# Optimization experiments

Hardware: AMD Instinct MI355X
Metric: run time of the kernel (lower is better)

The kernel has to match this reference:

```python
import jax, jax.numpy as jnp
import numpy as np

K = 40  # GravNetConv k (hardcoded in PFNet7.forward's conv1)

def lrelu(x):
    # LeakyReLU(negative_slope=0.5)
    return jnp.where(x >= 0, x, 0.5 * x)

def lin(x, W, b=None):
    y = x @ W
    return y + b if b is not None else y


def setup_inputs() -> dict:
    key = jax.random.key(0)
    ks = jax.random.split(key, 24)
    N = 16384
    inp = {}
    inp["x0"] = jax.random.normal(ks[0], (N, 12), jnp.float32)
    inp["ygen"] = jax.random.normal(ks[1], (N, 6), jnp.float32)
    inp["ycand"] = jax.random.normal(ks[2], (N, 6), jnp.float32)
    inp["ygen_id"] = jax.random.randint(ks[3], (N,), 0, 6)
    inp["ycand_id"] = jax.random.randint(ks[4], (N,), 0, 6)

    def lp(k, din, dout):  # torch Linear default init (uniform +/- 1/sqrt(fan_in))
        s = float(1.0 / np.sqrt(din))
        kw, kb = jax.random.split(k)
        W = jax.random.uniform(kw, (din, dout), jnp.float32, -s, s)
        b = jax.random.uniform(kb, (dout,), jnp.float32, -s, s)
        return W, b

    inp["n1W0"], inp["n1b0"] = lp(ks[5], 12, 64)
    inp["n1W1"], inp["n1b1"] = lp(ks[6], 64, 64)
    inp["n1W2"], inp["n1b2"] = lp(ks[7], 64, 12)
    # GravNetConv: lin_s (space, 8), lin_h (propagate, 22), lin_out (12 + 2*22 -> 64)
    inp["gWs"], inp["gbs"] = lp(ks[8], 12, 8)
    inp["gWh"], inp["gbh"] = lp(ks[9], 12, 22)
    inp["gWo"], inp["gbo"] = lp(ks[10], 56, 64)
    # GraphConv: lin_rel (with bias), lin_root (no bias, PyG convention)
    inp["c2Wrel"], inp["c2brel"] = lp(ks[11], 64, 64)
    inp["c2Wroot"] = lp(ks[12], 64, 64)[0]
    inp["n2W0"], inp["n2b0"] = lp(ks[13], 64, 126)
    inp["n2W1"], inp["n2b1"] = lp(ks[14], 126, 126)
    inp["n2W2"], inp["n2b2"] = lp(ks[15], 126, 126)
    inp["n2W3"], inp["n2b3"] = lp(ks[16], 126, 6)
    inp["n3W0"], inp["n3b0"] = lp(ks[17], 82, 126)
    inp["n3W1"], inp["n3b1"] = lp(ks[18], 126, 126)
    inp["n3W2"], inp["n3b2"] = lp(ks[19], 126, 126)
    inp["n3W3"], inp["n3b3"] = lp(ks[20], 126, 6)
    return inp


def reference(x0, ygen, ycand, ygen_id, ycand_id,
              n1W0, n1b0, n1W1, n1b1, n1W2, n1b2,
              gWs, gbs, gWh, gbh, gWo, gbo,
              c2Wrel, c2brel, c2Wroot,
              n2W0, n2b0, n2W1, n2b1, n2W2, n2b2, n2W3, n2b3,
              n3W0, n3b0, n3W1, n3b1, n3W2, n3b2, n3W3, n3b3):
    N = x0.shape[0]
    # nn1 encoder
    x = lrelu(lin(x0, n1W0, n1b0))
    x = lrelu(lin(x, n1W1, n1b1))
    x = lrelu(lin(x, n1W2, n1b2))            # [N,12]
    # ---- GravNetConv: dynamic kNN graph in learned 8-dim space ----
    s = lin(x, gWs, gbs)                     # [N,8] spatial coords
    h = lin(x, gWh, gbh)                     # [N,22] propagated features
    sq = jnp.sum(s * s, axis=1)
    d2 = sq[:, None] + sq[None, :] - 2.0 * (s @ s.T)   # [N,N] squared dists
    ar = jnp.arange(N)
    d2 = d2.at[ar, ar].set(jnp.inf)          # knn_graph loop=False: no self edges
    negd2, idx = jax.lax.top_k(-d2, K)       # [N,K] k nearest neighbors
    w = jnp.exp(10.0 * negd2)                # edge_weight = exp(-10 * d^2)
    msg = h[idx] * w[..., None]              # [N,K,22] gathered messages
    agg = jnp.concatenate([msg.mean(axis=1), msg.max(axis=1)], axis=-1)  # [N,44]
    x = lin(jnp.concatenate([agg, x], axis=-1), gWo, gbo)  # [N,64]
    # ---- GraphConv on the same kNN graph (add-aggregation, edge-weighted) ----
    nbr = jnp.sum(x[idx] * w[..., None], axis=1)  # [N,64]
    x = lin(nbr, c2Wrel, c2brel) + x @ c2Wroot     # [N,64]
    # nn2: class id head
    y = lrelu(lin(x, n2W0, n2b0))
    y = lrelu(lin(y, n2W1, n2b1))
    y = lrelu(lin(y, n2W2, n2b2))
    cand_ids = lrelu(lin(y, n2W3, n2b3))     # [N,6]
    z = jnp.concatenate([x, cand_ids, x0], axis=-1)  # [N,82]
    z = lrelu(lin(z, n3W0, n3b0))
    z = lrelu(lin(z, n3W1, n3b1))
    z = lrelu(lin(z, n3W2, n3b2))
    cand_p4 = lrelu(lin(z, n3W3, n3b3))      # [N,6]
    return (cand_ids, cand_p4, ygen_id, ygen, ycand_id, ycand)
```

## Files before the change

kernel.cpp:

```cpp
#include <hip/hip_runtime.h>
#include <math.h>

static constexpr int KNN = 40;

__device__ __forceinline__ float lrelu_f(float v){ return v >= 0.f ? v : 0.5f*v; }

typedef _Float16 half8 __attribute__((ext_vector_type(8)));
typedef float    f32x4 __attribute__((ext_vector_type(4)));

__device__ __forceinline__ void gload16(const void* g, void* l){
    __builtin_amdgcn_global_load_lds((const __attribute__((address_space(1))) void*)g,
                                     (__attribute__((address_space(3))) void*)l, 16, 0, 0);
}

#define PAD_OFF_GWS   0
#define PAD_OFF_GWH   192
#define PAD_OFF_N1W2  576
#define PAD_OFF_N2W3  1600
#define PAD_OFF_N3W3  3616
#define PAD_TOTAL     5632

#define T_N2W0  0
#define T_N2W1  8192
#define T_N2W2  24576
#define T_N3W0  40960
#define T_N3W1  53248
#define T_N3W2  69632
#define T_TOTAL 86016

__global__ void pad_all(const float* gWs,const float* gWh,const float* n1W2,
                        const float* n2W3,const float* n3W3,
                        const float* n2W0,const float* n2W1,const float* n2W2,
                        const float* n3W0,const float* n3W1,const float* n3W2,
                        float* __restrict__ wp, _Float16* __restrict__ wt)
{
    int i = blockIdx.x*blockDim.x + threadIdx.x;
    if (i < PAD_TOTAL) {
        const float* src; int cols, sh, off;
        if      (i < PAD_OFF_GWH)  { src=gWs;  cols=8;  sh=4; off=PAD_OFF_GWS;  }
        else if (i < PAD_OFF_N1W2) { src=gWh;  cols=22; sh=5; off=PAD_OFF_GWH;  }
        else if (i < PAD_OFF_N2W3) { src=n1W2; cols=12; sh=4; off=PAD_OFF_N1W2; }
        else if (i < PAD_OFF_N3W3) { src=n2W3; cols=6;  sh=4; off=PAD_OFF_N2W3; }
        else                       { src=n3W3; cols=6;  sh=4; off=PAD_OFF_N3W3; }
        int li = i - off;
        int r = li >> sh, c = li & ((1<<sh)-1);
        wp[i] = (c < cols) ? src[r*cols + c] : 0.f;
        return;
    }
    int j = i - PAD_TOTAL;
    if (j >= T_TOTAL) return;
    const float* src; int KP, K, off;
    if      (j < T_N2W1) { src=n2W0; KP=64;  K=64;  off=T_N2W0; }
    else if (j < T_N2W2) { src=n2W1; KP=128; K=126; off=T_N2W1; }
    else if (j < T_N3W0) { src=n2W2; KP=128; K=126; off=T_N2W2; }
    else if (j < T_N3W1) { src=n3W0; KP=96;  K=82;  off=T_N3W0; }
    else if (j < T_N3W2) { src=n3W1; KP=128; K=126; off=T_N3W1; }
    else                 { src=n3W2; KP=128; K=126; off=T_N3W2; }
    int li = j - off;
    int n = li / KP, k = li - n*KP;
    float v = (n < 126 && k < K) ? src[k*126 + n] : 0.f;
    wt[j] = (_Float16)v;
}

template<int K, int NOUT, int WPITCH, bool RELU, int NTH>
__device__ __forceinline__
void lin8(const float* __restrict__ Xs, int xpitch,
          const float* __restrict__ W, const float* __restrict__ Bv,
          float* __restrict__ Y, int ypitch, int tid)
{
    constexpr int NP  = ((NOUT+7)/8)*8;
    constexpr int NCG = NP/8;
    constexpr int NW  = NTH/64;
    const int lane = tid & 63;
    for (int g0 = tid >> 6; g0 < NCG; g0 += NW) {
        const int cg = __builtin_amdgcn_readfirstlane(g0);
        float acc[8];
        #pragma unroll
        for (int j=0;j<8;++j){ int c=cg*8+j; acc[j] = (c < NOUT) ? Bv[c] : 0.f; }
        const float* xrow = &Xs[(long)lane*xpitch];
        const float* wp = &W[cg*8];
        #pragma unroll 4
        for (int k=0;k<K;++k){
            const float xv = xrow[k];
            const float4* w4 = reinterpret_cast<const float4*>(wp + (long)k*WPITCH);
            float4 a = w4[0], b = w4[1];
            acc[0]=fmaf(xv,a.x,acc[0]); acc[1]=fmaf(xv,a.y,acc[1]);
            acc[2]=fmaf(xv,a.z,acc[2]); acc[3]=fmaf(xv,a.w,acc[3]);
            acc[4]=fmaf(xv,b.x,acc[4]); acc[5]=fmaf(xv,b.y,acc[5]);
            acc[6]=fmaf(xv,b.z,acc[6]); acc[7]=fmaf(xv,b.w,acc[7]);
        }
        #pragma unroll
        for (int j=0;j<8;++j){
            int c = cg*8 + j;
            if (c < NOUT){ float v = acc[j]; if (RELU) v = lrelu_f(v); Y[(long)lane*ypitch + c] = v; }
        }
    }
    __syncthreads();
}

template<int K, int NOUT, int WPITCH, int NTH>
__device__ __forceinline__
void lin8_dual(const float* __restrict__ Xs, int xp, const float* __restrict__ X2s, int xp2,
               const float* __restrict__ W, const float* __restrict__ Bv, const float* __restrict__ W2,
               float* __restrict__ Y, int ypitch, int tid)
{
    constexpr int NP  = ((NOUT+7)/8)*8;
    constexpr int NCG = NP/8;
    constexpr int NW  = NTH/64;
    const int lane = tid & 63;
    for (int g0 = tid >> 6; g0 < NCG; g0 += NW) {
        const int cg = __builtin_amdgcn_readfirstlane(g0);
        float acc[8];
        #pragma unroll
        for (int j=0;j<8;++j){ int c=cg*8+j; acc[j] = (c < NOUT) ? Bv[c] : 0.f; }
        {
            const float* xrow = &Xs[(long)lane*xp];
            const float* wp = &W[cg*8];
            #pragma unroll 4
            for (int k=0;k<K;++k){
                const float xv = xrow[k];
                const float4* w4 = reinterpret_cast<const float4*>(wp + (long)k*WPITCH);
                float4 a = w4[0], b = w4[1];
                acc[0]=fmaf(xv,a.x,acc[0]); acc[1]=fmaf(xv,a.y,acc[1]);
                acc[2]=fmaf(xv,a.z,acc[2]); acc[3]=fmaf(xv,a.w,acc[3]);
                acc[4]=fmaf(xv,b.x,acc[4]); acc[5]=fmaf(xv,b.y,acc[5]);
                acc[6]=fmaf(xv,b.z,acc[6]); acc[7]=fmaf(xv,b.w,acc[7]);
            }
        }
        {
            const float* xrow = &X2s[(long)lane*xp2];
            const float* wp = &W2[cg*8];
            #pragma unroll 4
            for (int k=0;k<K;++k){
                const float xv = xrow[k];
                const float4* w4 = reinterpret_cast<const float4*>(wp + (long)k*WPITCH);
                float4 a = w4[0], b = w4[1];
                acc[0]=fmaf(xv,a.x,acc[0]); acc[1]=fmaf(xv,a.y,acc[1]);
                acc[2]=fmaf(xv,a.z,acc[2]); acc[3]=fmaf(xv,a.w,acc[3]);
                acc[4]=fmaf(xv,b.x,acc[4]); acc[5]=fmaf(xv,b.y,acc[5]);
                acc[6]=fmaf(xv,b.z,acc[6]); acc[7]=fmaf(xv,b.w,acc[7]);
            }
        }
        #pragma unroll
        for (int j=0;j<8;++j){
            int c = cg*8 + j;
            if (c < NOUT) Y[(long)lane*ypitch + c] = acc[j];
        }
    }
    __syncthreads();
}

__global__ __launch_bounds__(512)
void f1_encoder(const float* __restrict__ x0, const float* __restrict__ wp,
                const float* n1W0,const float* n1b0,const float* n1W1,const float* n1b1,
                const float* n1b2, const float* gbs, const float* gbh,
                float* __restrict__ x12g,
                _Float16* __restrict__ SA16, _Float16* __restrict__ SB16 ,
                float* __restrict__ hg )
{
    __shared__ float A1[64*65], A2[64*65], Ss[64*9];
    const int tid = threadIdx.x;
    const long row0 = (long)blockIdx.x*64;
    lin8<12,64,64,true,512>(x0+row0*12,12, n1W0, n1b0, A1,65, tid);
    lin8<64,64,64,true,512>(A1,65, n1W1, n1b1, A2,65, tid);
    lin8<64,12,16,true,512>(A2,65, wp+PAD_OFF_N1W2, n1b2, A1,13, tid);
    for (int i=tid;i<64*12;i+=512){ int r=i/12,c=i-r*12; x12g[(row0+r)*12+c]=A1[r*13+c]; }
    lin8<12,8,16,false,512>(A1,13, wp+PAD_OFF_GWS, gbs, Ss,9, tid);
    lin8<12,22,32,false,512>(A1,13, wp+PAD_OFF_GWH, gbh, hg+row0*32,32, tid);
    if (tid < 64) {
        const long node = row0 + tid;
        float sv[8]; float nq = 0.f;
        #pragma unroll
        for (int k=0;k<8;++k){ float v=Ss[tid*9+k]; sv[k]=v; nq=fmaf(v,v,nq); }
        _Float16 ch[8], clo[8];
        #pragma unroll
        for (int k=0;k<8;++k){ ch[k]=(_Float16)sv[k]; clo[k]=(_Float16)(sv[k]-(float)ch[k]); }
        _Float16 nh = (_Float16)nq, nl = (_Float16)(nq-(float)nh);
        const _Float16 one = (_Float16)1.f, zero = (_Float16)0.f;
        half8 a0,a1,a2,b0,b2;
        #pragma unroll
        for (int k=0;k<8;++k){
            a0[k]=ch[k]; a1[k]=clo[k]; a2[k]=ch[k];
            b0[k]=(_Float16)(-2.f*(float)ch[k]);
            b2[k]=(_Float16)(-2.f*(float)clo[k]);
        }
        half8 a3 = {nh, nl, one, one, zero, zero, zero, zero};
        half8 b3 = {one, one, nh, nl, zero, zero, zero, zero};
        half8* ap = (half8*)&SA16[(size_t)node*32];
        ap[0]=a0; ap[1]=a1; ap[2]=a2; ap[3]=a3;
        half8* bp = (half8*)&SB16[(size_t)node*40];
        bp[0]=b0; bp[1]=b0; bp[2]=b2; bp[3]=b3;
        bp[4]=half8{zero,zero,zero,zero,zero,zero,zero,zero};
    }
}

template<int C>
__device__ __forceinline__ unsigned dpp_umin(unsigned x){
    unsigned y = (unsigned)__builtin_amdgcn_update_dpp((int)x, (int)x, C, 0xf, 0xf, false);
    return x < y ? x : y;
}
__device__ __forceinline__ unsigned wave_umin64(unsigned x){
    x = dpp_umin<0x111>(x);
    x = dpp_umin<0x112>(x);
    x = dpp_umin<0x114>(x);
    x = dpp_umin<0x118>(x);
    x = dpp_umin<0x142>(x);
    x = dpp_umin<0x143>(x);
    return x;
}
__device__ __forceinline__ unsigned med3_u32(unsigned a, unsigned b, unsigned c){
    unsigned d;
    asm("v_med3_u32 %0, %1, %2, %3" : "=v"(d) : "v"(a), "v"(b), "v"(c));
    return d;
}

__global__ __launch_bounds__(512)
void knn_scan(const _Float16* __restrict__ SA, const _Float16* __restrict__ SB,
              unsigned* __restrict__ part, int N)
{
    __shared__ __align__(16) _Float16 SBl[2][256*40];
    const int tid  = threadIdx.x;
    const int lane = tid & 63;
    const int w    = tid >> 6;
    const int g    = w >> 2, qt = w & 3;
    const int col  = lane & 15, kg = lane >> 4;
    const int qg   = blockIdx.x >> 1, half = blockIdx.x & 1;
    const int qb   = qg*32 + g*16;
    const int qtile = qb >> 8;
    const int rhs0  = (qb & 255) + kg*4;
    const int T0 = half*32;

    half8 afrag = *(const half8*)&SA[(size_t)(qb + col)*32 + kg*8];
    unsigned s0[4], s1[4];
    #pragma unroll
    for (int r=0;r<4;++r){ s0[r]=0xFFFFFFFFu; s1[r]=0xFFFFFFFFu; }

    {
        const char* gp = (const char*)(SB + (size_t)T0*256*40);
        gload16(gp + (size_t)tid*16,        &SBl[0][(size_t)tid*8]);
        gload16(gp + (size_t)(tid+512)*16,  &SBl[0][(size_t)(tid+512)*8]);
        if (tid < 256) gload16(gp + (size_t)(tid+1024)*16, &SBl[0][(size_t)(tid+1024)*8]);
    }
    __syncthreads();
    #pragma unroll 1
    for (int t = T0; t < T0+32; ++t) {
        const int cur = t & 1;
        if (t+1 < T0+32) {
            const char* gp = (const char*)(SB + (size_t)(t+1)*256*40);
            _Float16* lp = SBl[cur^1];
            gload16(gp + (size_t)tid*16,        &lp[(size_t)tid*8]);
            gload16(gp + (size_t)(tid+512)*16,  &lp[(size_t)(tid+512)*8]);
            if (tid < 256) gload16(gp + (size_t)(tid+1024)*16, &lp[(size_t)(tid+1024)*8]);
        }
        const _Float16* tb = SBl[cur];
        if (t != qtile) {
            #pragma unroll
            for (int c3=0;c3<4;++c3){
                const int cl_ = (qt*4+c3)*16 + col;
                half8 b = *(const half8*)&tb[cl_*40 + kg*8];
                f32x4 acc = {0.f,0.f,0.f,0.f};
                acc = __builtin_amdgcn_mfma_f32_16x16x32_f16(afrag, b, acc, 0, 0, 0);
                const unsigned ib = (unsigned)((t<<8)|cl_);
                #pragma unroll
                for (int r=0;r<4;++r){
                    float d2 = fmaxf(acc[r], 0.f);
                    unsigned key = (__float_as_uint(d2) & 0xFFFFC000u) | ib;
                    unsigned lo = s0[r] < key ? s0[r] : key;
                    s1[r] = med3_u32(s0[r], s1[r], key);
                    s0[r] = lo;
                }
            }
        } else {
            #pragma unroll
            for (int c3=0;c3<4;++c3){
                const int cl_ = (qt*4+c3)*16 + col;
                half8 b = *(const half8*)&tb[cl_*40 + kg*8];
                f32x4 acc = {0.f,0.f,0.f,0.f};
                acc = __builtin_amdgcn_mfma_f32_16x16x32_f16(afrag, b, acc, 0, 0, 0);
                const unsigned ib = (unsigned)((t<<8)|cl_);
                #pragma unroll
                for (int r=0;r<4;++r){
                    float d2 = fmaxf(acc[r], 0.f);
                    unsigned key = (__float_as_uint(d2) & 0xFFFFC000u) | ib;
                    if (cl_ == rhs0 + r) key = 0xFFFFFFFFu;
                    unsigned lo = s0[r] < key ? s0[r] : key;
                    s1[r] = med3_u32(s0[r], s1[r], key);
                    s0[r] = lo;
                }
            }
        }
        __syncthreads();
    }

    #pragma unroll
    for (int r=0;r<4;++r){
        const long q = (long)qg*32 + g*16 + kg*4 + r;
        unsigned* pp = &part[((size_t)q*2 + half)*128 + qt*32 + col*2];
        pp[0] = s0[r]; pp[1] = s1[r];
    }
}

__global__ __launch_bounds__(512)
void knn_merge(const unsigned* __restrict__ part,
               int* __restrict__ idx_out, float* __restrict__ w_out)
{
    const int lane = threadIdx.x & 63, w = threadIdx.x >> 6;
    const long q = (long)blockIdx.x*8 + w;
    const uint4 kk = *reinterpret_cast<const uint4*>(&part[(size_t)q*256 + lane*4]);
    unsigned k0=kk.x, k1=kk.y, k2=kk.z, k3=kk.w;
    unsigned saved = 0;
    #pragma unroll 1
    for (int p=0;p<KNN;++p){
        unsigned a = k0 < k1 ? k0 : k1;
        unsigned b = k2 < k3 ? k2 : k3;
        unsigned lmin = a < b ? a : b;
        unsigned red = wave_umin64(lmin);
        unsigned gm = (unsigned)__builtin_amdgcn_readlane((int)red, 63);
        unsigned long long bal = __ballot(lmin == gm);
        int owner = __ffsll((long long)bal) - 1;
        if (lane == owner){
            if      (k0 == gm) k0 = 0xFFFFFFFFu;
            else if (k1 == gm) k1 = 0xFFFFFFFFu;
            else if (k2 == gm) k2 = 0xFFFFFFFFu;
            else               k3 = 0xFFFFFFFFu;
        }
        if (lane == p) saved = gm;
    }
    if (lane < KNN){
        idx_out[q*KNN + lane] = (int)(saved & 16383u);
        const float d2 = __uint_as_float(saved & 0xFFFFC000u);
        w_out[q*KNN + lane] = expf(-10.f*d2);
    }
}

__global__ __launch_bounds__(512)
void f2_agg(const float* __restrict__ hg , const int* __restrict__ idx,
            const float* __restrict__ wgt, const float* __restrict__ x12g,
            const float* gWo, const float* gbo, float* __restrict__ xg)
{
    __shared__ int   IDs[64*40];
    __shared__ float Wt[64*40];
    __shared__ float AGG[64*57];
    const int tid = threadIdx.x;
    const long row0 = (long)blockIdx.x*64;
    for (int i=tid;i<64*40;i+=512){ int r=i/40,k=i-r*40;
        IDs[i]=idx[(row0+r)*40+k]; Wt[i]=wgt[(row0+r)*40+k]; }
    for (int i=tid;i<64*12;i+=512){ int r=i/12,c=i-r*12; AGG[r*57+44+c]=x12g[(row0+r)*12+c]; }
    __syncthreads();
    {
        const int r = tid & 63, g = tid >> 6;
        const int f0 = g*4;
        const int nf = (f0 < 22) ? ((22-f0) < 4 ? (22-f0) : 4) : 0;
        float sm[4], mx[4];
        #pragma unroll
        for (int u=0;u<4;++u){ sm[u]=0.f; mx[u]=-INFINITY; }
        if (nf > 0) {
            #pragma unroll 1
            for (int k=0;k<40;++k){
                int j = IDs[r*40+k]; float wv = Wt[r*40+k];
                float4 h0 = *reinterpret_cast<const float4*>(&hg[(long)j*32 + f0]);
                float hv[4] = {h0.x,h0.y,h0.z,h0.w};
                #pragma unroll
                for (int u=0;u<4;++u){ float m = hv[u]*wv; sm[u]+=m; mx[u]=fmaxf(mx[u],m); }
            }
            #pragma unroll
            for (int u=0;u<4;++u) if (u<nf){ AGG[r*57+f0+u]=sm[u]*(1.f/40.f); AGG[r*57+22+f0+u]=mx[u]; }
        }
    }
    __syncthreads();
    lin8<56,64,64,false,512>(AGG,57, gWo, gbo, xg+row0*64,64, tid);
}

template<int KP>
__device__ __forceinline__
void mfma_layer(const _Float16* __restrict__ Xl, const _Float16* __restrict__ WTg,
                _Float16* __restrict__ Wl,
                const float* __restrict__ Bv, _Float16* __restrict__ Yl, int tid)
{
    {
        const half8* src = reinterpret_cast<const half8*>(WTg);
        half8* dst = reinterpret_cast<half8*>(Wl);
        constexpr int CHUNKS = 128*KP/8;
        #pragma unroll
        for (int i = tid; i < CHUNKS; i += 1024) dst[i] = src[i];
    }
    __syncthreads();
    const int lane = tid & 63;
    const int wid  = __builtin_amdgcn_readfirstlane(tid >> 6);
    const int m   = wid & 3;
    const int nb  = wid >> 2;
    const int c15 = lane & 15;
    const int kg  = lane >> 4;
    f32x4 acc0 = {0.f,0.f,0.f,0.f};
    f32x4 acc1 = {0.f,0.f,0.f,0.f};
    const _Float16* xb = &Xl[(m*16 + c15)*136];
    const _Float16* w0 = &Wl[(nb*16 + c15)*KP];
    const _Float16* w1 = &Wl[((nb+4)*16 + c15)*KP];
    #pragma unroll
    for (int ks = 0; ks < KP/32; ++ks) {
        const int kb = kg*8 + ks*32;
        half8 a  = *reinterpret_cast<const half8*>(&xb[kb]);
        half8 b0 = *reinterpret_cast<const half8*>(&w0[kb]);
        half8 b1 = *reinterpret_cast<const half8*>(&w1[kb]);
        acc0 = __builtin_amdgcn_mfma_f32_16x16x32_f16(a, b0, acc0, 0, 0, 0);
        acc1 = __builtin_amdgcn_mfma_f32_16x16x32_f16(a, b1, acc1, 0, 0, 0);
    }
    const int drow = m*16 + kg*4;
    const int c0 = nb*16 + c15;
    const int c1 = (nb+4)*16 + c15;
    #pragma unroll
    for (int r = 0; r < 4; ++r) {
        float v0 = (c0 < 126) ? lrelu_f(acc0[r] + Bv[c0]) : 0.f;
        float v1 = (c1 < 126) ? lrelu_f(acc1[r] + Bv[c1]) : 0.f;
        Yl[(drow+r)*136 + c0] = (_Float16)v0;
        Yl[(drow+r)*136 + c1] = (_Float16)v1;
    }
    __syncthreads();
}

__device__ __forceinline__
void lin_out6h(const _Float16* __restrict__ Xs, const float* __restrict__ Wp,
               float* __restrict__ Wl6, const float* __restrict__ Bv,
               float* __restrict__ Y, int ypitch, int tid)
{
    for (int i = tid; i < 126*8; i += 1024) {
        int k = i >> 3, c = i & 7;
        Wl6[i] = Wp[k*16 + c];
    }
    __syncthreads();
    if (tid < 64*6) {
        const int r = tid / 6, c = tid - r*6;
        float acc = Bv[c];
        const _Float16* xrow = &Xs[r*136];
        #pragma unroll 4
        for (int k=0;k<126;++k) acc = fmaf((float)xrow[k], Wl6[k*8+c], acc);
        Y[(long)r*ypitch + c] = lrelu_f(acc);
    }
    __syncthreads();
}

__global__ __launch_bounds__(1024)
void f345(const float* __restrict__ xgin, const int* __restrict__ idx,
          const float* __restrict__ wgt,
          const float* c2Wrel, const float* c2brel, const float* c2Wroot,
          const float* __restrict__ x0,
          const float* __restrict__ wp, const _Float16* __restrict__ wt,
          const float* A_b0,const float* A_b1,const float* A_b2,const float* A_b3,
          const float* B_b0,const float* B_b1,const float* B_b2,const float* B_b3,
          float* __restrict__ outIds, float* __restrict__ outP4)
{
    __shared__ float XCs[64*65];
    __shared__ __align__(16) char uni[69120];
    int*   IDs = (int*)uni;
    float* Wt  = (float*)(uni+10240);
    float* NB  = (float*)(uni+20480);
    float* XGs = (float*)(uni+37120);
    _Float16* bufA = (_Float16*)uni;
    _Float16* bufB = (_Float16*)(uni+17408);
    _Float16* Wl   = (_Float16*)(uni+34816);
    float*    IDS6 = (float*)(uni+67584);

    const int tid = threadIdx.x;
    const long row0 = (long)blockIdx.x*64;
    for (int i=tid;i<64*40;i+=1024){ int r=i/40,k=i-r*40;
        IDs[i]=idx[(row0+r)*40+k]; Wt[i]=wgt[(row0+r)*40+k]; }
    for (int i=tid;i<64*64;i+=1024){ int r=i>>6,c=i&63; XGs[r*65+c]=xgin[(row0+r)*64+c]; }
    __syncthreads();
    {
        const int r = tid & 63, g = tid >> 6;
        float acc[4] = {0.f,0.f,0.f,0.f};
        #pragma unroll 1
        for (int k=0;k<40;++k){
            int j = IDs[r*40+k]; float wv = Wt[r*40+k];
            float4 v = *reinterpret_cast<const float4*>(&xgin[(long)j*64 + g*4]);
            acc[0]=fmaf(v.x,wv,acc[0]); acc[1]=fmaf(v.y,wv,acc[1]);
            acc[2]=fmaf(v.z,wv,acc[2]); acc[3]=fmaf(v.w,wv,acc[3]);
        }
        __syncthreads();
        #pragma unroll
        for (int j=0;j<4;++j) NB[r*65 + g*4 + j] = acc[j];
    }
    __syncthreads();
    lin8_dual<64,64,64,1024>(NB,65, XGs,65, c2Wrel,c2brel,c2Wroot, XCs,65, tid);
    for (int i=tid;i<64*64;i+=1024){ int r=i>>6,c=i&63;
        bufA[r*136+c] = (_Float16)XCs[r*65+c]; }
    __syncthreads();
    mfma_layer<64>(bufA, wt+T_N2W0, Wl, A_b0, bufB, tid);
    mfma_layer<128>(bufB, wt+T_N2W1, Wl, A_b1, bufA, tid);
    mfma_layer<128>(bufA, wt+T_N2W2, Wl, A_b2, bufB, tid);
    lin_out6h(bufB, wp+PAD_OFF_N2W3, (float*)Wl, A_b3, IDS6, 6, tid);
    for (int i=tid;i<64*6;i+=1024){ int r=i/6,c=i-r*6; outIds[(row0+r)*6+c]=IDS6[i]; }
    for (int i=tid;i<64*96;i+=1024){
        int r=i/96, c=i-r*96;
        float v;
        if (c < 64)      v = XCs[r*65 + c];
        else if (c < 70) v = IDS6[r*6 + (c-64)];
        else if (c < 82) v = x0[(row0+r)*12 + (c-70)];
        else             v = 0.f;
        bufA[r*136+c] = (_Float16)v;
    }
    __syncthreads();
    mfma_layer<96>(bufA, wt+T_N3W0, Wl, B_b0, bufB, tid);
    mfma_layer<128>(bufB, wt+T_N3W1, Wl, B_b1, bufA, tid);
    mfma_layer<128>(bufA, wt+T_N3W2, Wl, B_b2, bufB, tid);
    lin_out6h(bufB, wp+PAD_OFF_N3W3, (float*)Wl, B_b3, outP4+row0*6, 6, tid);
}

__global__ void copyout_kernel(const int* __restrict__ gid, const float* __restrict__ gy,
                               const int* __restrict__ cid, const float* __restrict__ cy,
                               float* __restrict__ out, int N)
{
    long i = (long)blockIdx.x*blockDim.x + threadIdx.x;
    long n = N;
    if (i < n)            out[12*n + i]         = (float)gid[i];
    else if (i < 7*n)     out[13*n + (i - n)]   = gy[i - n];
    else if (i < 8*n)     out[19*n + (i - 7*n)] = (float)cid[i - 7*n];
    else if (i < 14*n)    out[20*n + (i - 8*n)] = cy[i - 8*n];
}

extern "C" void kernel_launch(void* const* d_in, const int* in_sizes, int n_in,
                              void* d_out, int out_size, void* d_ws, size_t ws_size,
                              hipStream_t stream)
{
    const float* x0     = (const float*)d_in[0];
    const float* ygen   = (const float*)d_in[1];
    const float* ycand  = (const float*)d_in[2];
    const int*   ygenid = (const int*)d_in[3];
    const int*   ycandid= (const int*)d_in[4];
    const float* n1W0=(const float*)d_in[5],  *n1b0=(const float*)d_in[6];
    const float* n1W1=(const float*)d_in[7],  *n1b1=(const float*)d_in[8];
    const float* n1W2=(const float*)d_in[9],  *n1b2=(const float*)d_in[10];
    const float* gWs =(const float*)d_in[11], *gbs =(const float*)d_in[12];
    const float* gWh =(const float*)d_in[13], *gbh =(const float*)d_in[14];
    const float* gWo =(const float*)d_in[15], *gbo =(const float*)d_in[16];
    const float* c2Wrel=(const float*)d_in[17], *c2brel=(const float*)d_in[18];
    const float* c2Wroot=(const float*)d_in[19];
    const float* n2W0=(const float*)d_in[20], *n2b0=(const float*)d_in[21];
    const float* n2W1=(const float*)d_in[22], *n2b1=(const float*)d_in[23];
    const float* n2W2=(const float*)d_in[24], *n2b2=(const float*)d_in[25];
    const float* n2W3=(const float*)d_in[26], *n2b3=(const float*)d_in[27];
    const float* n3W0=(const float*)d_in[28], *n3b0=(const float*)d_in[29];
    const float* n3W1=(const float*)d_in[30], *n3b1=(const float*)d_in[31];
    const float* n3W2=(const float*)d_in[32], *n3b2=(const float*)d_in[33];
    const float* n3W3=(const float*)d_in[34], *n3b3=(const float*)d_in[35];

    const int N = in_sizes[0] / 12;
    float* ws = (float*)d_ws;
    size_t off = 0;
    auto alloc = [&](size_t cnt){ float* p = ws + off; off += cnt; return p; };
    float* padw = alloc(PAD_TOTAL);
    _Float16* wt16 = (_Float16*)alloc((T_TOTAL+1)/2 + 8);
    float* x12  = alloc((size_t)N*12);
    _Float16* SA16 = (_Float16*)alloc((size_t)N*16);
    _Float16* SB16 = (_Float16*)alloc((size_t)N*20);
    float* h    = alloc((size_t)N*32);
    unsigned* part = (unsigned*)alloc((size_t)N*256);
    int*   idxb = (int*)alloc((size_t)N*KNN);
    float* wb   = alloc((size_t)N*KNN);
    float* xg   = alloc((size_t)N*64);
    (void)ws_size; (void)n_in; (void)out_size;

    float* outF = (float*)d_out;
    const int GB = N / 64;

    pad_all<<<(PAD_TOTAL+T_TOTAL+255)/256,256,0,stream>>>(gWs,gWh,n1W2,n2W3,n3W3,
                                                          n2W0,n2W1,n2W2,n3W0,n3W1,n3W2,
                                                          padw, wt16);
    f1_encoder<<<GB,512,0,stream>>>(x0, padw, n1W0,n1b0, n1W1,n1b1, n1b2,
                                    gbs, gbh, x12, SA16, SB16, h);
    knn_scan<<<(N/32)*2, 512, 0, stream>>>(SA16, SB16, part, N);
    knn_merge<<<N/8, 512, 0, stream>>>(part, idxb, wb);
    f2_agg<<<GB,512,0,stream>>>(h, idxb, wb, x12, gWo, gbo, xg);
    f345<<<GB,1024,0,stream>>>(xg, idxb, wb, c2Wrel, c2brel, c2Wroot, x0, padw, wt16,
                               n2b0,n2b1,n2b2,n2b3, n3b0,n3b1,n3b2,n3b3,
                               outF, outF + (size_t)N*6);
    copyout_kernel<<<(14*N+255)/256,256,0,stream>>>(ygenid, ygen, ycandid, ycand, outF, N);
}
```

Before: 204.4 us.

## Shrink f345 blocks to 32 rows with 512 threads and remap all stages

New measurement: 210.0 us. 2.7% more time.

```diff
diff --git a/kernel.cpp b/kernel.cpp
--- a/kernel.cpp
+++ b/kernel.cpp
@@ -98,55 +98,44 @@
     __syncthreads();
 }
 
-template<int K, int NOUT, int WPITCH, int NTH>
+template<int K, int WPITCH>
 __device__ __forceinline__
-void lin8_dual(const float* __restrict__ Xs, int xp, const float* __restrict__ X2s, int xp2,
-               const float* __restrict__ W, const float* __restrict__ Bv, const float* __restrict__ W2,
-               float* __restrict__ Y, int ypitch, int tid)
-{
-    constexpr int NP  = ((NOUT+7)/8)*8;
-    constexpr int NCG = NP/8;
-    constexpr int NW  = NTH/64;
+void lin4_dual_32(const float* __restrict__ Xs, int xp, const float* __restrict__ X2s, int xp2,
+                  const float* __restrict__ W, const float* __restrict__ Bv, const float* __restrict__ W2,
+                  float* __restrict__ Y, int ypitch, int tid)
+{
     const int lane = tid & 63;
-    for (int g0 = tid >> 6; g0 < NCG; g0 += NW) {
-        const int cg = __builtin_amdgcn_readfirstlane(g0);
-        float acc[8];
-        #pragma unroll
-        for (int j=0;j<8;++j){ int c=cg*8+j; acc[j] = (c < NOUT) ? Bv[c] : 0.f; }
-        {
-            const float* xrow = &Xs[(long)lane*xp];
-            const float* wp = &W[cg*8];
-            #pragma unroll 4
-            for (int k=0;k<K;++k){
-                const float xv = xrow[k];
-                const float4* w4 = reinterpret_cast<const float4*>(wp + (long)k*WPITCH);
-                float4 a = w4[0], b = w4[1];
-                acc[0]=fmaf(xv,a.x,acc[0]); acc[1]=fmaf(xv,a.y,acc[1]);
-                acc[2]=fmaf(xv,a.z,acc[2]); acc[3]=fmaf(xv,a.w,acc[3]);
-                acc[4]=fmaf(xv,b.x,acc[4]); acc[5]=fmaf(xv,b.y,acc[5]);
-                acc[6]=fmaf(xv,b.z,acc[6]); acc[7]=fmaf(xv,b.w,acc[7]);
-            }
-        }
-        {
-            const float* xrow = &X2s[(long)lane*xp2];
-            const float* wp = &W2[cg*8];
-            #pragma unroll 4
-            for (int k=0;k<K;++k){
-                const float xv = xrow[k];
-                const float4* w4 = reinterpret_cast<const float4*>(wp + (long)k*WPITCH);
-                float4 a = w4[0], b = w4[1];
-                acc[0]=fmaf(xv,a.x,acc[0]); acc[1]=fmaf(xv,a.y,acc[1]);
-                acc[2]=fmaf(xv,a.z,acc[2]); acc[3]=fmaf(xv,a.w,acc[3]);
-                acc[4]=fmaf(xv,b.x,acc[4]); acc[5]=fmaf(xv,b.y,acc[5]);
-                acc[6]=fmaf(xv,b.z,acc[6]); acc[7]=fmaf(xv,b.w,acc[7]);
-            }
-        }
-        #pragma unroll
-        for (int j=0;j<8;++j){
-            int c = cg*8 + j;
-            if (c < NOUT) Y[(long)lane*ypitch + c] = acc[j];
-        }
-    }
+    const int w    = tid >> 6;
+    const int r    = lane & 31;
+    const int h    = lane >> 5;
+    const int c0   = w*8 + h*4;
+    float acc[4];
+    #pragma unroll
+    for (int j=0;j<4;++j) acc[j] = Bv[c0+j];
+    {
+        const float* xrow = &Xs[(long)r*xp];
+        const float* wp = &W[c0];
+        #pragma unroll 4
+        for (int k=0;k<K;++k){
+            const float xv = xrow[k];
+            float4 a = *reinterpret_cast<const float4*>(wp + (long)k*WPITCH);
+            acc[0]=fmaf(xv,a.x,acc[0]); acc[1]=fmaf(xv,a.y,acc[1]);
+            acc[2]=fmaf(xv,a.z,acc[2]); acc[3]=fmaf(xv,a.w,acc[3]);
+        }
+    }
+    {
+        const float* xrow = &X2s[(long)r*xp2];
+        const float* wp = &W2[c0];
+        #pragma unroll 4
+        for (int k=0;k<K;++k){
+            const float xv = xrow[k];
+            float4 a = *reinterpret_cast<const float4*>(wp + (long)k*WPITCH);
+            acc[0]=fmaf(xv,a.x,acc[0]); acc[1]=fmaf(xv,a.y,acc[1]);
+            acc[2]=fmaf(xv,a.z,acc[2]); acc[3]=fmaf(xv,a.w,acc[3]);
+        }
+    }
+    #pragma unroll
+    for (int j=0;j<4;++j) Y[(long)r*ypitch + c0 + j] = acc[j];
     __syncthreads();
 }
 
@@ -373,22 +362,22 @@
 
 template<int KP>
 __device__ __forceinline__
-void mfma_layer(const _Float16* __restrict__ Xl, const _Float16* __restrict__ WTg,
-                _Float16* __restrict__ Wl,
-                const float* __restrict__ Bv, _Float16* __restrict__ Yl, int tid)
+void mfma_layer32(const _Float16* __restrict__ Xl, const _Float16* __restrict__ WTg,
+                  _Float16* __restrict__ Wl,
+                  const float* __restrict__ Bv, _Float16* __restrict__ Yl, int tid)
 {
     {
         const half8* src = reinterpret_cast<const half8*>(WTg);
         half8* dst = reinterpret_cast<half8*>(Wl);
         constexpr int CHUNKS = 128*KP/8;
         #pragma unroll
-        for (int i = tid; i < CHUNKS; i += 1024) dst[i] = src[i];
+        for (int i = tid; i < CHUNKS; i += 512) dst[i] = src[i];
     }
     __syncthreads();
     const int lane = tid & 63;
     const int wid  = __builtin_amdgcn_readfirstlane(tid >> 6);
-    const int m   = wid & 3;
-    const int nb  = wid >> 2;
+    const int m   = wid & 1;
+    const int nb  = wid >> 1;
     const int c15 = lane & 15;
     const int kg  = lane >> 4;
     f32x4 acc0 = {0.f,0.f,0.f,0.f};
@@ -419,16 +408,16 @@
 }
 
 __device__ __forceinline__
-void lin_out6h(const _Float16* __restrict__ Xs, const float* __restrict__ Wp,
-               float* __restrict__ Wl6, const float* __restrict__ Bv,
-               float* __restrict__ Y, int ypitch, int tid)
-{
-    for (int i = tid; i < 126*8; i += 1024) {
+void lin_out6h32(const _Float16* __restrict__ Xs, const float* __restrict__ Wp,
+                 float* __restrict__ Wl6, const float* __restrict__ Bv,
+                 float* __restrict__ Y, int ypitch, int tid)
+{
+    for (int i = tid; i < 126*8; i += 512) {
         int k = i >> 3, c = i & 7;
         Wl6[i] = Wp[k*16 + c];
     }
     __syncthreads();
-    if (tid < 64*6) {
+    if (tid < 32*6) {
         const int r = tid / 6, c = tid - r*6;
         float acc = Bv[c];
         const _Float16* xrow = &Xs[r*136];
@@ -439,7 +428,7 @@
     __syncthreads();
 }
 
-__global__ __launch_bounds__(1024)
+__global__ __launch_bounds__(512)
 void f345(const float* __restrict__ xgin, const int* __restrict__ idx,
           const float* __restrict__ wgt,
           const float* c2Wrel, const float* c2brel, const float* c2Wroot,
@@ -449,25 +438,25 @@
           const float* B_b0,const float* B_b1,const float* B_b2,const float* B_b3,
           float* __restrict__ outIds, float* __restrict__ outP4)
 {
-    __shared__ float XCs[64*65];
-    __shared__ __align__(16) char uni[69120];
+    __shared__ float XCs[32*65];
+    __shared__ __align__(16) char uni[50944];
     int*   IDs = (int*)uni;
-    float* Wt  = (float*)(uni+10240);
-    float* NB  = (float*)(uni+20480);
-    float* XGs = (float*)(uni+37120);
+    float* Wt  = (float*)(uni+5120);
+    float* NB  = (float*)(uni+10240);
+    float* XGs = (float*)(uni+18560);
     _Float16* bufA = (_Float16*)uni;
-    _Float16* bufB = (_Float16*)(uni+17408);
-    _Float16* Wl   = (_Float16*)(uni+34816);
-    float*    IDS6 = (float*)(uni+67584);
+    _Float16* bufB = (_Float16*)(uni+8704);
+    _Float16* Wl   = (_Float16*)(uni+17408);
+    float*    IDS6 = (float*)(uni+50176);
 
     const int tid = threadIdx.x;
-    const long row0 = (long)blockIdx.x*64;
-    for (int i=tid;i<64*40;i+=1024){ int r=i/40,k=i-r*40;
+    const long row0 = (long)blockIdx.x*32;
+    for (int i=tid;i<32*40;i+=512){ int r=i/40,k=i-r*40;
         IDs[i]=idx[(row0+r)*40+k]; Wt[i]=wgt[(row0+r)*40+k]; }
-    for (int i=tid;i<64*64;i+=1024){ int r=i>>6,c=i&63; XGs[r*65+c]=xgin[(row0+r)*64+c]; }
+    for (int i=tid;i<32*64;i+=512){ int r=i>>6,c=i&63; XGs[r*65+c]=xgin[(row0+r)*64+c]; }
     __syncthreads();
     {
-        const int r = tid & 63, g = tid >> 6;
+        const int r = tid & 31, g = tid >> 5;
         float acc[4] = {0.f,0.f,0.f,0.f};
         #pragma unroll 1
         for (int k=0;k<40;++k){
@@ -481,16 +470,16 @@
         for (int j=0;j<4;++j) NB[r*65 + g*4 + j] = acc[j];
     }
     __syncthreads();
-    lin8_dual<64,64,64,1024>(NB,65, XGs,65, c2Wrel,c2brel,c2Wroot, XCs,65, tid);
-    for (int i=tid;i<64*64;i+=1024){ int r=i>>6,c=i&63;
+    lin4_dual_32<64,64>(NB,65, XGs,65, c2Wrel,c2brel,c2Wroot, XCs,65, tid);
+    for (int i=tid;i<32*64;i+=512){ int r=i>>6,c=i&63;
         bufA[r*136+c] = (_Float16)XCs[r*65+c]; }
     __syncthreads();
-    mfma_layer<64>(bufA, wt+T_N2W0, Wl, A_b0, bufB, tid);
-    mfma_layer<128>(bufB, wt+T_N2W1, Wl, A_b1, bufA, tid);
-    mfma_layer<128>(bufA, wt+T_N2W2, Wl, A_b2, bufB, tid);
-    lin_out6h(bufB, wp+PAD_OFF_N2W3, (float*)Wl, A_b3, IDS6, 6, tid);
-    for (int i=tid;i<64*6;i+=1024){ int r=i/6,c=i-r*6; outIds[(row0+r)*6+c]=IDS6[i]; }
-    for (int i=tid;i<64*96;i+=1024){
+    mfma_layer32<64>(bufA, wt+T_N2W0, Wl, A_b0, bufB, tid);
+    mfma_layer32<128>(bufB, wt+T_N2W1, Wl, A_b1, bufA, tid);
+    mfma_layer32<128>(bufA, wt+T_N2W2, Wl, A_b2, bufB, tid);
+    lin_out6h32(bufB, wp+PAD_OFF_N2W3, (float*)Wl, A_b3, IDS6, 6, tid);
+    for (int i=tid;i<32*6;i+=512){ int r=i/6,c=i-r*6; outIds[(row0+r)*6+c]=IDS6[i]; }
+    for (int i=tid;i<32*96;i+=512){
         int r=i/96, c=i-r*96;
         float v;
         if (c < 64)      v = XCs[r*65 + c];
@@ -500,10 +489,10 @@
         bufA[r*136+c] = (_Float16)v;
     }
     __syncthreads();
-    mfma_layer<96>(bufA, wt+T_N3W0, Wl, B_b0, bufB, tid);
-    mfma_layer<128>(bufB, wt+T_N3W1, Wl, B_b1, bufA, tid);
-    mfma_layer<128>(bufA, wt+T_N3W2, Wl, B_b2, bufB, tid);
-    lin_out6h(bufB, wp+PAD_OFF_N3W3, (float*)Wl, B_b3, outP4+row0*6, 6, tid);
+    mfma_layer32<96>(bufA, wt+T_N3W0, Wl, B_b0, bufB, tid);
+    mfma_layer32<128>(bufB, wt+T_N3W1, Wl, B_b1, bufA, tid);
+    mfma_layer32<128>(bufA, wt+T_N3W2, Wl, B_b2, bufB, tid);
+    lin_out6h32(bufB, wp+PAD_OFF_N3W3, (float*)Wl, B_b3, outP4+row0*6, 6, tid);
 }
 
 __global__ void copyout_kernel(const int* __restrict__ gid, const float* __restrict__ gy,
@@ -571,8 +560,8 @@
     knn_scan<<<(N/32)*2, 512, 0, stream>>>(SA16, SB16, part, N);
     knn_merge<<<N/8, 512, 0, stream>>>(part, idxb, wb);
     f2_agg<<<GB,512,0,stream>>>(h, idxb, wb, x12, gWo, gbo, xg);
-    f345<<<GB,1024,0,stream>>>(xg, idxb, wb, c2Wrel, c2brel, c2Wroot, x0, padw, wt16,
-                               n2b0,n2b1,n2b2,n2b3, n3b0,n3b1,n3b2,n3b3,
-                               outF, outF + (size_t)N*6);
+    f345<<<N/32,512,0,stream>>>(xg, idxb, wb, c2Wrel, c2brel, c2Wroot, x0, padw, wt16,
+                                n2b0,n2b1,n2b2,n2b3, n3b0,n3b1,n3b2,n3b3,
+                                outF, outF + (size_t)N*6);
     copyout_kernel<<<(14*N+255)/256,256,0,stream>>>(ygenid, ygen, ycandid, ycand, outF, N);
 }
```
